# Performance work log

Measured on AMD Instinct MI355X. Metric: run time of the kernel, lower is better.

The kernel has to match this reference:

```python
import jax, jax.numpy as jnp
import numpy as np

B, N, M = 8, 4096, 77
Q_DIM, CTX_DIM = 1024, 768
H, D = 16, 64
INNER = H * D  # 1024


def setup_inputs() -> dict:
    key = jax.random.key(0)
    ks = jax.random.split(key, 7)
    x = jax.random.normal(ks[0], (B, N, Q_DIM), dtype=jnp.float32)
    context = jax.random.normal(ks[1], (B, M, CTX_DIM), dtype=jnp.float32)
    # Linear weights stored as [in, out] so y = x @ W (no bias for q/k/v).
    Wq = jax.random.normal(ks[2], (Q_DIM, INNER), dtype=jnp.float32) * (Q_DIM ** -0.5)
    Wk = jax.random.normal(ks[3], (CTX_DIM, INNER), dtype=jnp.float32) * (CTX_DIM ** -0.5)
    Wv = jax.random.normal(ks[4], (CTX_DIM, INNER), dtype=jnp.float32) * (CTX_DIM ** -0.5)
    Wo = jax.random.normal(ks[5], (INNER, Q_DIM), dtype=jnp.float32) * (INNER ** -0.5)
    bo = jax.random.normal(ks[6], (Q_DIM,), dtype=jnp.float32) * 0.01
    return {"x": x, "context": context, "Wq": Wq, "Wk": Wk, "Wv": Wv, "Wo": Wo, "bo": bo}


def reference(x, context, Wq, Wk, Wv, Wo, bo):
    scale = D ** -0.5
    # Project and split heads: [B, S, H*D] -> [B, H, S, D]
    def heads(t):
        b, s, _ = t.shape
        return t.reshape(b, s, H, D).transpose(0, 2, 1, 3)
    q = heads(x @ Wq)        # [B, H, N, D]
    k = heads(context @ Wk)  # [B, H, M, D]
    v = heads(context @ Wv)  # [B, H, M, D]
    scores = jnp.einsum('bhid,bhjd->bhij', q, k) * scale  # [B, H, N, M]
    attn = jax.nn.softmax(scores, axis=-1)
    out = jnp.einsum('bhij,bhjd->bhid', attn, v)          # [B, H, N, D]
    out = out.transpose(0, 2, 1, 3).reshape(x.shape[0], x.shape[1], INNER)
    return out @ Wo + bo  # dropout p=0.0 -> identity
```

## Files before the change

### kernel.cpp

```cpp
#include <hip/hip_runtime.h>
#include <hip/hip_bf16.h>

typedef _Float16 f16x8 __attribute__((ext_vector_type(8)));
typedef float f32x4 __attribute__((ext_vector_type(4)));

#define MFMA16(a, b, c) __builtin_amdgcn_mfma_f32_16x16x32_f16(a, b, c, 0, 0, 0)

__device__ __forceinline__ void load_lds16(const void* g, void* l) {
  __builtin_amdgcn_global_load_lds(
      (__attribute__((address_space(1))) void*)g,
      (__attribute__((address_space(3))) void*)l, 16, 0, 0);
}

__global__ __launch_bounds__(256) void k_prep(const float* __restrict__ x,
                                              const float* __restrict__ ctx,
                                              const float* __restrict__ Wq,
                                              const float* __restrict__ Wk,
                                              const float* __restrict__ Wv,
                                              const float* __restrict__ Wo,
                                              _Float16* __restrict__ xh,
                                              _Float16* __restrict__ ctxh,
                                              _Float16* __restrict__ Wqt,
                                              _Float16* __restrict__ Wkt,
                                              _Float16* __restrict__ Wvt,
                                              _Float16* __restrict__ Wot,
                                              _Float16* __restrict__ Vtg) {
  __shared__ float tile[64][65];
  const int b = blockIdx.x, t = threadIdx.x;

  if (b < 4096) {
    for (int i = b * 256 + t; i < 4194304; i += 4096 * 256) {
      const float4* p = (const float4*)(x + (size_t)i * 8);
      float4 a = p[0], c = p[1];
      f16x8 v = {(_Float16)a.x, (_Float16)a.y, (_Float16)a.z, (_Float16)a.w,
                 (_Float16)c.x, (_Float16)c.y, (_Float16)c.z, (_Float16)c.w};
      *(f16x8*)(xh + (size_t)i * 8) = v;
    }
    return;
  }
  if (b < 4327) {
    int i = (b - 4096) * 256 + t;
    const float4* p = (const float4*)(ctx + (size_t)i * 8);
    float4 a = p[0], c = p[1];
    f16x8 v = {(_Float16)a.x, (_Float16)a.y, (_Float16)a.z, (_Float16)a.w,
               (_Float16)c.x, (_Float16)c.y, (_Float16)c.z, (_Float16)c.w};
    *(f16x8*)(ctxh + (size_t)i * 8) = v;
    return;
  }
  if (b >= 5223) {
    int i = (b - 5223) * 256 + t;
    ((f16x8*)Vtg)[i] = f16x8{};
    return;
  }
  const float* tin;
  _Float16* tout;
  int TK, TN, i;
  if (b < 4583)      { tin = Wq; tout = Wqt; TK = 1024; TN = 1024; i = b - 4327; }
  else if (b < 4775) { tin = Wk; tout = Wkt; TK = 768;  TN = 1024; i = b - 4583; }
  else if (b < 4967) { tin = Wv; tout = Wvt; TK = 768;  TN = 1024; i = b - 4775; }
  else               { tin = Wo; tout = Wot; TK = 1024; TN = 1024; i = b - 4967; }
  int n0 = (i & 15) * 64, k0 = (i >> 4) * 64;
  {
    int nn = t & 63, kb = t >> 6;
#pragma unroll
    for (int s = 0; s < 16; ++s) {
      int kk = kb + s * 4;
      tile[kk][nn] = tin[(size_t)(k0 + kk) * TN + n0 + nn];
    }
  }
  __syncthreads();
  {
    int kk = t & 63, nb = t >> 6;
#pragma unroll
    for (int s = 0; s < 16; ++s) {
      int nn = nb + s * 4;
      tout[(size_t)(n0 + nn) * TK + k0 + kk] = (_Float16)tile[kk][nn];
    }
  }
}

__global__ __launch_bounds__(64) void k_kvproj(const _Float16* __restrict__ ctxh,
                                               const _Float16* __restrict__ Wkt,
                                               const _Float16* __restrict__ Wvt,
                                               _Float16* __restrict__ Kg,
                                               _Float16* __restrict__ Vtg) {
  int mt = blockIdx.x, nt = blockIdx.y;
  int lane = threadIdx.x;
  int l15 = lane & 15, lhi = lane >> 4;
  int arow = mt * 16 + l15;
  if (arow > 615) arow = 615;
  const _Float16* ap = ctxh + (size_t)arow * 768 + lhi * 8;
  const _Float16* kp = Wkt + (size_t)(nt * 16 + l15) * 768 + lhi * 8;
  const _Float16* vp = Wvt + (size_t)(nt * 16 + l15) * 768 + lhi * 8;
  f32x4 ak = {0.f, 0.f, 0.f, 0.f}, av = {0.f, 0.f, 0.f, 0.f};
#pragma unroll 4
  for (int ks = 0; ks < 24; ++ks) {
    f16x8 a = *(const f16x8*)(ap + ks * 32);
    f16x8 bk = *(const f16x8*)(kp + ks * 32);
    f16x8 bv = *(const f16x8*)(vp + ks * 32);
    ak = MFMA16(a, bk, ak);
    av = MFMA16(a, bv, av);
  }
  int n = nt * 16 + l15, h = n >> 6, d = n & 63;
#pragma unroll
  for (int j = 0; j < 4; ++j) {
    int gm = mt * 16 + lhi * 4 + j;
    if (gm < 616) {
      int b = gm / 77, m = gm - b * 77;
      Kg[((size_t)(b * 16 + h) * 77 + m) * 64 + d] = (_Float16)ak[j];
      Vtg[((size_t)(b * 16 + h) * 64 + d) * 128 + m] = (_Float16)av[j];
    }
  }
}

template <int MODE>
__global__ __launch_bounds__(512, 2) void k_gemm9(const _Float16* __restrict__ A,
                                                  const _Float16* __restrict__ Bt,
                                                  void* __restrict__ Cout,
                                                  const float* __restrict__ bias,
                                                  const _Float16* __restrict__ Kg,
                                                  const _Float16* __restrict__ Vtg,
                                                  int M, int N, int K) {
  __shared__ __align__(16) char lds[MODE == 0 ? 163840 : 131072];
  const int t = threadIdx.x, wid = t >> 6, lane = t & 63;
  const int wr = wid >> 2, wc = wid & 3;
  const int l15 = lane & 15, lhi = lane >> 4;

  int nwg = gridDim.x, bid = blockIdx.x;
  int wg = ((nwg & 7) == 0) ? ((bid & 7) * (nwg >> 3) + (bid >> 3)) : bid;
  const int nTN = N >> 8;
  const int tm = wg / nTN, tn = wg % nTN;

  const _Float16* Ag = A + (size_t)tm * 256 * K;
  const _Float16* Bg = Bt + (size_t)tn * 256 * K;
  const size_t stg = (size_t)(wid * 8 + (lane >> 3)) * K +
                     (size_t)(((lane & 7) ^ ((lane >> 3) & 7)) * 8);
  const int dstg = wid * 1024;

  const int x7 = l15 & 7;
  const int cs0 = (lhi ^ x7) << 4;
  const int cs1 = ((4 + lhi) ^ x7) << 4;
  const int aoff = wr * 16384 + l15 * 128;
  const int boff = 32768 + wc * 8192 + l15 * 128;

  f32x4 acc[8][4];
#pragma unroll
  for (int i = 0; i < 8; ++i)
#pragma unroll
    for (int j = 0; j < 4; ++j) acc[i][j] = f32x4{0.f, 0.f, 0.f, 0.f};
  f16x8 a0k0[4], a0k1[4], a1k0[4], a1k1[4];
  f16x8 b00[2], b01[2], b10[2], b11[2];

#define STG_A(T, RB) load_lds16(Ag + stg + (size_t)(RB) * K + (T) * 64, \
                                lds + ((T) & 1) * 65536 + (RB) * 128 + dstg)
#define STG_B(T, RB) load_lds16(Bg + stg + (size_t)(RB) * K + (T) * 64, \
                                lds + ((T) & 1) * 65536 + 32768 + (RB) * 128 + dstg)
#define STG_TILE(T) { STG_A(T, 0); STG_A(T, 64); STG_A(T, 128); STG_A(T, 192);  \
                      STG_B(T, 0); STG_B(T, 64); STG_B(T, 128); STG_B(T, 192); }
#define RDA(DST, BUF, MH, CS) { const int p_ = (BUF) * 65536 + aoff + (MH) * 8192; \
    _Pragma("unroll") for (int mf = 0; mf < 4; ++mf)                               \
      DST[mf] = *(const f16x8*)&lds[p_ + mf * 2048 + (CS)]; }
#define RDB(DST, BUF, NH, CS) { const int q_ = (BUF) * 65536 + boff + (NH) * 4096; \
    _Pragma("unroll") for (int nf = 0; nf < 2; ++nf)                               \
      DST[nf] = *(const f16x8*)&lds[q_ + nf * 2048 + (CS)]; }
#define MMC(MH, NH, AR, BR) { __builtin_amdgcn_s_setprio(1);                       \
    _Pragma("unroll") for (int mf = 0; mf < 4; ++mf)                               \
      _Pragma("unroll") for (int nf = 0; nf < 2; ++nf)                             \
        acc[(MH)*4+mf][(NH)*2+nf] = MFMA16(AR[mf], BR[nf],                         \
                                           acc[(MH)*4+mf][(NH)*2+nf]);             \
    __builtin_amdgcn_s_setprio(0); }
#define VM0 asm volatile("s_waitcnt vmcnt(0)" ::: "memory")
#define BAR __builtin_amdgcn_s_barrier()

#define TILE(BUF, T, STG_ON)                                                       \
  {                                                                                \
    VM0; BAR;                                                                      \
    RDA(a0k0, BUF, 0, cs0); RDB(b00, BUF, 0, cs0);                                 \
    RDB(b10, BUF, 1, cs0);                                                         \
    if (STG_ON) STG_TILE((T) + 1);                                                 \
    MMC(0, 0, a0k0, b00);                                                          \
    RDA(a1k0, BUF, 1, cs0); MMC(0, 1, a0k0, b10);                                  \
    RDA(a1k1, BUF, 1, cs1); MMC(1, 1, a1k0, b10);                                  \
    RDB(b01, BUF, 0, cs1);  MMC(1, 0, a1k0, b00);                                  \
    RDB(b11, BUF, 1, cs1);  MMC(1, 0, a1k1, b01);                                  \
    RDA(a0k1, BUF, 0, cs1); MMC(1, 1, a1k1, b11);                                  \
    MMC(0, 1, a0k1, b11);                                                          \
    MMC(0, 0, a0k1, b01);                                                          \
  }

  const int nT = K >> 6;

  STG_TILE(0);

  for (int i = 0; i < (nT >> 1) - 1; ++i) {
    TILE(0, 2 * i, true);
    TILE(1, 2 * i + 1, true);
  }
  TILE(0, nT - 2, true);
  TILE(1, nT - 1, false);

  if (MODE == 1) {
    const long rbase = (long)tm * 256 + wr * 128;
    const int cbase = tn * 256 + wc * 64;
#pragma unroll
    for (int mf = 0; mf < 8; ++mf)
#pragma unroll
      for (int nf = 0; nf < 4; ++nf) {
        int c = cbase + nf * 16 + l15;
        float bv = bias[c];
#pragma unroll
        for (int j = 0; j < 4; ++j) {
          long r = rbase + mf * 16 + lhi * 4 + j;
          ((float*)Cout)[r * N + c] = acc[mf][nf][j] + bv;
        }
      }
    return;
  }

  BAR;

  const int h = tn * 4 + wc;
  const int bh = (tm >> 4) * 16 + h;
  const _Float16* Kgp = Kg + (size_t)bh * (77 * 64);
  const _Float16* Vgp = Vtg + (size_t)bh * (64 * 128);

  f16x8 kf[5][2];
#pragma unroll
  for (int ct = 0; ct < 5; ++ct) {
    int m = ct * 16 + l15;
    kf[ct][0] = *(const f16x8*)(Kgp + m * 64 + lhi * 8);
    kf[ct][1] = *(const f16x8*)(Kgp + m * 64 + 32 + lhi * 8);
  }
  f16x8 vf[3][4];
#pragma unroll
  for (int ks = 0; ks < 3; ++ks)
#pragma unroll
    for (int dt = 0; dt < 4; ++dt) {
      int d = dt * 16 + l15;
      vf[ks][dt] = *(const f16x8*)(Vgp + d * 128 + ks * 32 + lhi * 8);
    }

  const int qbase = wid * 16384;
#pragma unroll
  for (int mf = 0; mf < 8; ++mf)
#pragma unroll
    for (int nf = 0; nf < 4; ++nf)
#pragma unroll
      for (int j = 0; j < 4; ++j) {
        int row = mf * 16 + lhi * 4 + j;
        int d = nf * 16 + l15;
        int by = (row * 128 + d * 2) ^ ((row & 7) << 4);
        *(_Float16*)&lds[qbase + by] = (_Float16)acc[mf][nf][j];
      }

  const int pbase = 131072 + wid * 4096;
#pragma unroll
  for (int i = 0; i < 4; ++i)
    *(f16x8*)&lds[pbase + lane * 64 + i * 16] = f16x8{};

  const long orow0 = (long)tm * 256 + wr * 128;
  _Float16* aOut = (_Float16*)Cout;

  for (int mf = 0; mf < 8; ++mf) {
    const int qm = qbase + mf * 2048 + l15 * 128;
    f16x8 q0 = *(const f16x8*)&lds[qm + cs0];
    f16x8 q1 = *(const f16x8*)&lds[qm + cs1];

    float e[5][4];
    float mx[4] = {-1e30f, -1e30f, -1e30f, -1e30f};
    __builtin_amdgcn_s_setprio(1);
#pragma unroll
    for (int ct = 0; ct < 5; ++ct) {
      f32x4 s = {0.f, 0.f, 0.f, 0.f};
      s = MFMA16(q0, kf[ct][0], s);
      s = MFMA16(q1, kf[ct][1], s);
      bool valid = (ct * 16 + l15) < 77;
#pragma unroll
      for (int j = 0; j < 4; ++j) {
        float v = valid ? s[j] * 0.125f : -1e30f;
        e[ct][j] = v;
        mx[j] = fmaxf(mx[j], v);
      }
    }
    __builtin_amdgcn_s_setprio(0);
#pragma unroll
    for (int off = 1; off < 16; off <<= 1)
#pragma unroll
      for (int j = 0; j < 4; ++j) mx[j] = fmaxf(mx[j], __shfl_xor(mx[j], off, 64));

    float sm[4] = {0.f, 0.f, 0.f, 0.f};
#pragma unroll
    for (int ct = 0; ct < 5; ++ct)
#pragma unroll
      for (int j = 0; j < 4; ++j) {
        float ev = __expf(e[ct][j] - mx[j]);
        e[ct][j] = ev;
        sm[j] += ev;
      }
#pragma unroll
    for (int ct = 0; ct < 5; ++ct) {
      int m = ct * 16 + l15;
#pragma unroll
      for (int j = 0; j < 4; ++j) {
        int r = lhi * 4 + j;
        *(_Float16*)&lds[pbase + ((r * 256 + m * 2) ^ ((r & 7) << 4))] =
            (_Float16)e[ct][j];
      }
    }
#pragma unroll
    for (int off = 1; off < 16; off <<= 1)
#pragma unroll
      for (int j = 0; j < 4; ++j) sm[j] += __shfl_xor(sm[j], off, 64);
    float rs[4];
#pragma unroll
    for (int j = 0; j < 4; ++j) rs[j] = 1.0f / sm[j];

    f32x4 o[4] = {{0.f,0.f,0.f,0.f},{0.f,0.f,0.f,0.f},{0.f,0.f,0.f,0.f},{0.f,0.f,0.f,0.f}};
    __builtin_amdgcn_s_setprio(1);
#pragma unroll
    for (int ks = 0; ks < 3; ++ks) {
      int m0b = ks * 64 + lhi * 16;
      f16x8 pa = *(const f16x8*)&lds[pbase + ((l15 * 256 + m0b) ^ ((l15 & 7) << 4))];
#pragma unroll
      for (int dt = 0; dt < 4; ++dt)
        o[dt] = MFMA16(pa, vf[ks][dt], o[dt]);
    }
    __builtin_amdgcn_s_setprio(0);
    _Float16* op = aOut + (size_t)(orow0 + mf * 16 + lhi * 4) * 1024 + h * 64;
#pragma unroll
    for (int dt = 0; dt < 4; ++dt)
#pragma unroll
      for (int j = 0; j < 4; ++j)
        op[(size_t)j * 1024 + dt * 16 + l15] = (_Float16)(o[dt][j] * rs[j]);
  }
#undef STG_A
#undef STG_B
#undef STG_TILE
#undef RDA
#undef RDB
#undef MMC
#undef TILE
#undef VM0
#undef BAR
}

extern "C" void kernel_launch(void* const* d_in, const int* in_sizes, int n_in,
                              void* d_out, int out_size, void* d_ws, size_t ws_size,
                              hipStream_t stream) {
  const float* x   = (const float*)d_in[0];
  const float* ctx = (const float*)d_in[1];
  const float* Wq  = (const float*)d_in[2];
  const float* Wk  = (const float*)d_in[3];
  const float* Wv  = (const float*)d_in[4];
  const float* Wo  = (const float*)d_in[5];
  const float* bo  = (const float*)d_in[6];

  char* ws = (char*)d_ws;
  _Float16* xh   = (_Float16*)(ws + 0);
  _Float16* Wqt  = (_Float16*)(ws + 67108864);
  _Float16* Wkt  = (_Float16*)(ws + 69206016);
  _Float16* Wvt  = (_Float16*)(ws + 70778880);
  _Float16* Wot  = (_Float16*)(ws + 72351744);
  _Float16* ctxh = (_Float16*)(ws + 74448896);
  _Float16* Kg   = (_Float16*)(ws + 75395072);
  _Float16* Vtg  = (_Float16*)(ws + 76656640);
  _Float16* aOut = (_Float16*)(ws + 78774272);

  k_prep<<<5735, 256, 0, stream>>>(x, ctx, Wq, Wk, Wv, Wo,
                                   xh, ctxh, Wqt, Wkt, Wvt, Wot, Vtg);
  k_kvproj<<<dim3(39, 64), 64, 0, stream>>>(ctxh, Wkt, Wvt, Kg, Vtg);
  k_gemm9<0><<<dim3(512), dim3(512), 0, stream>>>(xh, Wqt, (void*)aOut, nullptr,
                                                  Kg, Vtg, 32768, 1024, 1024);
  k_gemm9<1><<<dim3(512), dim3(512), 0, stream>>>(aOut, Wot, d_out, bo,
                                                  nullptr, nullptr, 32768, 1024, 1024);
}
```

Measured before the change: 243.0 us.

## Shrink GEMM tile to 128x256 with triple-buffered LDS pipeline

Halves the M tile of both fused GEMM kernels from 256 to 128 rows, doubling the grid to 1024 workgroups and shrinking per-wave accumulators. The K loop now uses three LDS buffers with a two-tile-ahead prefetch and a partial vmcnt wait, replacing the double-buffered interleaved read/MFMA schedule. The aim is better load overlap and more workgroups to balance across CUs. In exchange, arithmetic intensity per tile drops, so the B operand is reloaded twice as often. The LDS footprint of 144KB may also limit occupancy.

```diff
diff --git a/kernel.cpp b/kernel.cpp
--- a/kernel.cpp
+++ b/kernel.cpp
@@ -114,14 +114,14 @@
 }
 
 template <int MODE>
-__global__ __launch_bounds__(512, 2) void k_gemm9(const _Float16* __restrict__ A,
+__global__ __launch_bounds__(512, 2) void k_gemmR(const _Float16* __restrict__ A,
                                                   const _Float16* __restrict__ Bt,
                                                   void* __restrict__ Cout,
                                                   const float* __restrict__ bias,
                                                   const _Float16* __restrict__ Kg,
                                                   const _Float16* __restrict__ Vtg,
                                                   int M, int N, int K) {
-  __shared__ __align__(16) char lds[MODE == 0 ? 163840 : 131072];
+  __shared__ __align__(16) char lds[147456];
   const int t = threadIdx.x, wid = t >> 6, lane = t & 63;
   const int wr = wid >> 2, wc = wid & 3;
   const int l15 = lane & 15, lhi = lane >> 4;
@@ -131,7 +131,7 @@
   const int nTN = N >> 8;
   const int tm = wg / nTN, tn = wg % nTN;
 
-  const _Float16* Ag = A + (size_t)tm * 256 * K;
+  const _Float16* Ag = A + (size_t)tm * 128 * K;
   const _Float16* Bg = Bt + (size_t)tn * 256 * K;
   const size_t stg = (size_t)(wid * 8 + (lane >> 3)) * K +
                      (size_t)(((lane & 7) ^ ((lane >> 3) & 7)) * 8);
@@ -140,70 +140,72 @@
   const int x7 = l15 & 7;
   const int cs0 = (lhi ^ x7) << 4;
   const int cs1 = ((4 + lhi) ^ x7) << 4;
-  const int aoff = wr * 16384 + l15 * 128;
-  const int boff = 32768 + wc * 8192 + l15 * 128;
-
-  f32x4 acc[8][4];
-#pragma unroll
-  for (int i = 0; i < 8; ++i)
+  const int aoff = (wr * 64 + l15) * 128;
+  const int boff = 16384 + (wc * 64 + l15) * 128;
+
+  f32x4 acc[4][4];
+#pragma unroll
+  for (int i = 0; i < 4; ++i)
 #pragma unroll
     for (int j = 0; j < 4; ++j) acc[i][j] = f32x4{0.f, 0.f, 0.f, 0.f};
-  f16x8 a0k0[4], a0k1[4], a1k0[4], a1k1[4];
-  f16x8 b00[2], b01[2], b10[2], b11[2];
-
-#define STG_A(T, RB) load_lds16(Ag + stg + (size_t)(RB) * K + (T) * 64, \
-                                lds + ((T) & 1) * 65536 + (RB) * 128 + dstg)
-#define STG_B(T, RB) load_lds16(Bg + stg + (size_t)(RB) * K + (T) * 64, \
-                                lds + ((T) & 1) * 65536 + 32768 + (RB) * 128 + dstg)
-#define STG_TILE(T) { STG_A(T, 0); STG_A(T, 64); STG_A(T, 128); STG_A(T, 192);  \
-                      STG_B(T, 0); STG_B(T, 64); STG_B(T, 128); STG_B(T, 192); }
-#define RDA(DST, BUF, MH, CS) { const int p_ = (BUF) * 65536 + aoff + (MH) * 8192; \
-    _Pragma("unroll") for (int mf = 0; mf < 4; ++mf)                               \
-      DST[mf] = *(const f16x8*)&lds[p_ + mf * 2048 + (CS)]; }
-#define RDB(DST, BUF, NH, CS) { const int q_ = (BUF) * 65536 + boff + (NH) * 4096; \
-    _Pragma("unroll") for (int nf = 0; nf < 2; ++nf)                               \
-      DST[nf] = *(const f16x8*)&lds[q_ + nf * 2048 + (CS)]; }
-#define MMC(MH, NH, AR, BR) { __builtin_amdgcn_s_setprio(1);                       \
-    _Pragma("unroll") for (int mf = 0; mf < 4; ++mf)                               \
-      _Pragma("unroll") for (int nf = 0; nf < 2; ++nf)                             \
-        acc[(MH)*4+mf][(NH)*2+nf] = MFMA16(AR[mf], BR[nf],                         \
-                                           acc[(MH)*4+mf][(NH)*2+nf]);             \
-    __builtin_amdgcn_s_setprio(0); }
+  f16x8 a0[4], a1[4], b0[4], b1[4];
+
+#define STG_TILE(T, BUF)                                                          \
+  {                                                                               \
+    const size_t co = (size_t)(T) * 64;                                           \
+    char* d_ = lds + (BUF) * 49152 + dstg;                                        \
+    load_lds16(Ag + stg + co, d_);                                                \
+    load_lds16(Ag + stg + (size_t)64 * K + co, d_ + 8192);                        \
+    load_lds16(Bg + stg + co, d_ + 16384);                                        \
+    load_lds16(Bg + stg + (size_t)64 * K + co, d_ + 16384 + 8192);                \
+    load_lds16(Bg + stg + (size_t)128 * K + co, d_ + 16384 + 16384);              \
+    load_lds16(Bg + stg + (size_t)192 * K + co, d_ + 16384 + 24576);              \
+  }
+#define VM6 asm volatile("s_waitcnt vmcnt(6)" ::: "memory")
 #define VM0 asm volatile("s_waitcnt vmcnt(0)" ::: "memory")
 #define BAR __builtin_amdgcn_s_barrier()
 
-#define TILE(BUF, T, STG_ON)                                                       \
-  {                                                                                \
-    VM0; BAR;                                                                      \
-    RDA(a0k0, BUF, 0, cs0); RDB(b00, BUF, 0, cs0);                                 \
-    RDB(b10, BUF, 1, cs0);                                                         \
-    if (STG_ON) STG_TILE((T) + 1);                                                 \
-    MMC(0, 0, a0k0, b00);                                                          \
-    RDA(a1k0, BUF, 1, cs0); MMC(0, 1, a0k0, b10);                                  \
-    RDA(a1k1, BUF, 1, cs1); MMC(1, 1, a1k0, b10);                                  \
-    RDB(b01, BUF, 0, cs1);  MMC(1, 0, a1k0, b00);                                  \
-    RDB(b11, BUF, 1, cs1);  MMC(1, 0, a1k1, b01);                                  \
-    RDA(a0k1, BUF, 0, cs1); MMC(1, 1, a1k1, b11);                                  \
-    MMC(0, 1, a0k1, b11);                                                          \
-    MMC(0, 0, a0k1, b01);                                                          \
-  }
-
   const int nT = K >> 6;
 
-  STG_TILE(0);
-
-  for (int i = 0; i < (nT >> 1) - 1; ++i) {
-    TILE(0, 2 * i, true);
-    TILE(1, 2 * i + 1, true);
-  }
-  TILE(0, nT - 2, true);
-  TILE(1, nT - 1, false);
+  STG_TILE(0, 0);
+  STG_TILE(1, 1);
+
+  int bufR = 0;
+  for (int tt = 0; tt < nT; ++tt) {
+    if (tt == nT - 1) { VM0; } else { VM6; }
+    BAR;
+    if (tt < nT - 2) {
+      int bufS = bufR + 2; if (bufS >= 3) bufS -= 3;
+      STG_TILE(tt + 2, bufS);
+    }
+    const int base = bufR * 49152;
+#pragma unroll
+    for (int mf = 0; mf < 4; ++mf) {
+      a0[mf] = *(const f16x8*)&lds[base + aoff + mf * 2048 + cs0];
+      a1[mf] = *(const f16x8*)&lds[base + aoff + mf * 2048 + cs1];
+    }
+#pragma unroll
+    for (int nf = 0; nf < 4; ++nf) {
+      b0[nf] = *(const f16x8*)&lds[base + boff + nf * 2048 + cs0];
+      b1[nf] = *(const f16x8*)&lds[base + boff + nf * 2048 + cs1];
+    }
+    __builtin_amdgcn_s_setprio(1);
+#pragma unroll
+    for (int mf = 0; mf < 4; ++mf)
+#pragma unroll
+      for (int nf = 0; nf < 4; ++nf) {
+        acc[mf][nf] = MFMA16(a0[mf], b0[nf], acc[mf][nf]);
+        acc[mf][nf] = MFMA16(a1[mf], b1[nf], acc[mf][nf]);
+      }
+    __builtin_amdgcn_s_setprio(0);
+    bufR = (bufR == 2) ? 0 : bufR + 1;
+  }
 
   if (MODE == 1) {
-    const long rbase = (long)tm * 256 + wr * 128;
+    const long rbase = (long)tm * 128 + wr * 64;
     const int cbase = tn * 256 + wc * 64;
 #pragma unroll
-    for (int mf = 0; mf < 8; ++mf)
+    for (int mf = 0; mf < 4; ++mf)
 #pragma unroll
       for (int nf = 0; nf < 4; ++nf) {
         int c = cbase + nf * 16 + l15;
@@ -220,7 +222,7 @@
   BAR;
 
   const int h = tn * 4 + wc;
-  const int bh = (tm >> 4) * 16 + h;
+  const int bh = (tm >> 5) * 16 + h;
   const _Float16* Kgp = Kg + (size_t)bh * (77 * 64);
   const _Float16* Vgp = Vtg + (size_t)bh * (64 * 128);
 
@@ -240,9 +242,9 @@
       vf[ks][dt] = *(const f16x8*)(Vgp + d * 128 + ks * 32 + lhi * 8);
     }
 
-  const int qbase = wid * 16384;
-#pragma unroll
-  for (int mf = 0; mf < 8; ++mf)
+  const int qbase = wid * 8192;
+#pragma unroll
+  for (int mf = 0; mf < 4; ++mf)
 #pragma unroll
     for (int nf = 0; nf < 4; ++nf)
 #pragma unroll
@@ -253,15 +255,15 @@
         *(_Float16*)&lds[qbase + by] = (_Float16)acc[mf][nf][j];
       }
 
-  const int pbase = 131072 + wid * 4096;
+  const int pbase = 65536 + wid * 4096;
 #pragma unroll
   for (int i = 0; i < 4; ++i)
     *(f16x8*)&lds[pbase + lane * 64 + i * 16] = f16x8{};
 
-  const long orow0 = (long)tm * 256 + wr * 128;
+  const long orow0 = (long)tm * 128 + wr * 64;
   _Float16* aOut = (_Float16*)Cout;
 
-  for (int mf = 0; mf < 8; ++mf) {
+  for (int mf = 0; mf < 4; ++mf) {
     const int qm = qbase + mf * 2048 + l15 * 128;
     f16x8 q0 = *(const f16x8*)&lds[qm + cs0];
     f16x8 q1 = *(const f16x8*)&lds[qm + cs1];
@@ -333,13 +335,8 @@
       for (int j = 0; j < 4; ++j)
         op[(size_t)j * 1024 + dt * 16 + l15] = (_Float16)(o[dt][j] * rs[j]);
   }
-#undef STG_A
-#undef STG_B
 #undef STG_TILE
-#undef RDA
-#undef RDB
-#undef MMC
-#undef TILE
+#undef VM6
 #undef VM0
 #undef BAR
 }
@@ -369,8 +366,8 @@
   k_prep<<<5735, 256, 0, stream>>>(x, ctx, Wq, Wk, Wv, Wo,
                                    xh, ctxh, Wqt, Wkt, Wvt, Wot, Vtg);
   k_kvproj<<<dim3(39, 64), 64, 0, stream>>>(ctxh, Wkt, Wvt, Kg, Vtg);
-  k_gemm9<0><<<dim3(512), dim3(512), 0, stream>>>(xh, Wqt, (void*)aOut, nullptr,
-                                                  Kg, Vtg, 32768, 1024, 1024);
-  k_gemm9<1><<<dim3(512), dim3(512), 0, stream>>>(aOut, Wot, d_out, bo,
-                                                  nullptr, nullptr, 32768, 1024, 1024);
-}
+  k_gemmR<0><<<dim3(1024), dim3(512), 0, stream>>>(xh, Wqt, (void*)aOut, nullptr,
+                                                   Kg, Vtg, 32768, 1024, 1024);
+  k_gemmR<1><<<dim3(1024), dim3(512), 0, stream>>>(aOut, Wot, d_out, bo,
+                                                   nullptr, nullptr, 32768, 1024, 1024);
+}
```

Measured after the change: 274.3 us. 1.13x slower.
